# Performance work log

Hardware: AMD Instinct MI355X
Metric: run time of the kernel (lower is better)

Reference implementation:

```python
import jax, jax.numpy as jnp
import numpy as np

B, T, N = 4, 512, 16
D, H = 256, 8
CTS, CN, CE = 6, 4, 3
TSE, AUXE = 192, 64  # TSE + AUXE == D
DK = D // H


def pe_table(L, d):
    # sinusoidal positional encoding (annotated-transformer style)
    pos = jnp.arange(L, dtype=jnp.float32)[:, None]
    div = jnp.exp(jnp.arange(0, d, 2, dtype=jnp.float32) * (-jnp.log(jnp.float32(10000.0)) / d))
    pe = jnp.zeros((L, d), dtype=jnp.float32)
    pe = pe.at[:, 0::2].set(jnp.sin(pos * div)).at[:, 1::2].set(jnp.cos(pos * div))
    return pe


def setup_inputs() -> dict:
    key = jax.random.key(0)
    ks = jax.random.split(key, 32)
    s = 0.02
    inp = {
        'x': jax.random.normal(ks[0], (B, T, D), jnp.float32),
        'masked_data': jax.random.normal(ks[1], (B, N, CTS, T), jnp.float32),
        'node_aux': jax.random.normal(ks[2], (B, N, CN, T), jnp.float32),
        'edge_aux': jax.random.normal(ks[3], (B, N, CE, T), jnp.float32),
        'attention_mask': jax.random.randint(ks[4], (B, T, N * T), 0, 2, jnp.int32),
        # ts branch
        'W_ts1': jax.random.normal(ks[5], (CTS, TSE)) * s, 'b_ts1': jnp.zeros((TSE,)),
        'W_ts2': jax.random.normal(ks[6], (TSE, TSE)) * s, 'b_ts2': jnp.zeros((TSE,)),
        # node aux branch
        'W_a1': jax.random.normal(ks[7], (CN, AUXE)) * s, 'b_a1': jnp.zeros((AUXE,)),
        'W_a2': jax.random.normal(ks[8], (AUXE, AUXE)) * s, 'b_a2': jnp.zeros((AUXE,)),
        # edge branch
        'W_e1': jax.random.normal(ks[9], (CE, D)) * s, 'b_e1': jnp.zeros((D,)),
        'W_e2': jax.random.normal(ks[10], (D, D)) * s, 'b_e2': jnp.zeros((D,)),
        # multi-head cross-attention
        'Wq': jax.random.normal(ks[11], (D, D)) * s, 'bq': jnp.zeros((D,)),
        'Wk': jax.random.normal(ks[12], (D, D)) * s, 'bk': jnp.zeros((D,)),
        'Wv': jax.random.normal(ks[13], (D, D)) * s, 'bv': jnp.zeros((D,)),
        'Wo': jax.random.normal(ks[14], (D, D)) * s, 'bo': jnp.zeros((D,)),
        # sublayer layernorm
        'ln_g': jnp.ones((D,)), 'ln_b': jnp.zeros((D,)),
    }
    return inp


def reference(x, masked_data, node_aux, edge_aux, attention_mask,
              W_ts1, b_ts1, W_ts2, b_ts2, W_a1, b_a1, W_a2, b_a2,
              W_e1, b_e1, W_e2, b_e2, Wq, bq, Wk, bk, Wv, bv, Wo, bo,
              ln_g, ln_b):
    pe = pe_table(T, D)  # [T, D]
    xq = x + pe[None]  # pe applied to query sequence (dropout=identity in eval)

    # per-neighbor ts MLP: transpose [B,N,C,T] -> [B,N,T,C], two Linears with ReLU between
    ts = jax.nn.relu(jnp.einsum('bnct,ce->bnte', masked_data, W_ts1) + b_ts1)
    ts = ts @ W_ts2 + b_ts2  # [B,N,T,TSE]
    aux = jax.nn.relu(jnp.einsum('bnct,ce->bnte', node_aux, W_a1) + b_a1)
    aux = aux @ W_a2 + b_a2  # [B,N,T,AUXE]
    nbr = jnp.concatenate([ts, aux], axis=-1)  # [B,N,T,D]

    edge = jax.nn.relu(jnp.einsum('bnct,cd->bntd', edge_aux, W_e1) + b_e1)
    edge = edge @ W_e2 + b_e2  # [B,N,T,D]

    # PE applied per neighbor (positions restart each neighbor), then concat over kv seq
    keys = (nbr * edge + pe[None, None]).reshape(B, N * T, D)
    vals = (nbr + pe[None, None]).reshape(B, N * T, D)

    # SublayerConnection: xq + attn(LayerNorm(xq), keys, vals, mask)
    mu = xq.mean(-1, keepdims=True)
    var = ((xq - mu) ** 2).mean(-1, keepdims=True)
    xn = (xq - mu) / jnp.sqrt(var + 1e-6) * ln_g + ln_b

    q = (xn @ Wq + bq).reshape(B, T, H, DK).transpose(0, 2, 1, 3)        # [B,H,T,DK]
    k = (keys @ Wk + bk).reshape(B, N * T, H, DK).transpose(0, 2, 1, 3)  # [B,H,NT,DK]
    v = (vals @ Wv + bv).reshape(B, N * T, H, DK).transpose(0, 2, 1, 3)

    scores = jnp.einsum('bhqd,bhkd->bhqk', q, k) / jnp.sqrt(jnp.float32(DK))
    scores = jnp.where(attention_mask[:, None, :, :] == 0, jnp.float32(-1e9), scores)
    attn = jax.nn.softmax(scores, axis=-1)
    ctx = jnp.einsum('bhqk,bhkd->bhqd', attn, v).transpose(0, 2, 1, 3).reshape(B, T, D)
    out = ctx @ Wo + bo
    return xq + out
```

## Files before the change

kernel.cpp:

```cpp
#include <hip/hip_runtime.h>
#include <hip/hip_bf16.h>

#define B_ 4
#define T_ 512
#define N_ 16
#define D_ 256
#define H_ 8
#define DK_ 32
#define NT_ (N_ * T_)
#define CTS_ 6
#define CN_ 4
#define CE_ 3
#define TSE_ 192
#define AUXE_ 64
#define SPLIT_ 8
#define KWORDS_ (NT_ / 64)

#define QSCALE_ 0.1767766952966369f

#define HTS_S 204
#define HAUX_S 76
#define HED_S 268
#define SK_S 268

typedef unsigned long long ull;
typedef unsigned int uint;
typedef __bf16 bf16x8 __attribute__((ext_vector_type(8)));
typedef float f32x4 __attribute__((ext_vector_type(4)));
typedef float f32x16 __attribute__((ext_vector_type(16)));

__global__ __launch_bounds__(256) void pe_kernel(float* pe) {
    int t = blockIdx.x;
    int d = threadIdx.x;
    int j = d >> 1;
    float div = expf((float)(2 * j) * (-9.210340371976184f / 256.0f));
    float a = (float)t * div;
    pe[t * D_ + d] = (d & 1) ? cosf(a) : sinf(a);
}

__global__ __launch_bounds__(256) void maskbits_kernel(const int* __restrict__ mask,
                                                       ull* __restrict__ bitsT) {
    int row = blockIdx.x;
    int b = row >> 9, t = row & (T_ - 1);
    const int* mrow = mask + (size_t)row * NT_;
    int lane = threadIdx.x & 63, wave = threadIdx.x >> 6;
    for (int it = 0; it < NT_ / 256; ++it) {
        int k = it * 256 + wave * 64 + lane;
        ull bal = __ballot(mrow[k] != 0);
        if (lane == 0) bitsT[((size_t)b * KWORDS_ + (k >> 6)) * T_ + t] = bal;
    }
}

__global__ __launch_bounds__(256) void wprep_kernel(
    const float* __restrict__ W_ts1, const float* __restrict__ W_a1,
    const float* __restrict__ W_e1, const float* __restrict__ W_ts2,
    const float* __restrict__ W_a2, const float* __restrict__ W_e2,
    const float* __restrict__ Wk, const float* __restrict__ Wv,
    const float* __restrict__ Wq, const float* __restrict__ Wo,
    __bf16* __restrict__ ts1P, __bf16* __restrict__ a1P, __bf16* __restrict__ e1P,
    __bf16* __restrict__ ts2T, __bf16* __restrict__ a2T, __bf16* __restrict__ e2T,
    __bf16* __restrict__ WkT, __bf16* __restrict__ WvT,
    __bf16* __restrict__ WqT, __bf16* __restrict__ WoT) {
    int i = blockIdx.x * 256 + threadIdx.x;
    if (i < 6144) { int col = i >> 5, k = i & 31;
        ts1P[i] = (__bf16)(k < 6 ? W_ts1[k * TSE_ + col] : 0.f); return; }
    i -= 6144;
    if (i < 2048) { int col = i >> 5, k = i & 31;
        a1P[i] = (__bf16)((k >= 6 && k < 10) ? W_a1[(k - 6) * AUXE_ + col] : 0.f); return; }
    i -= 2048;
    if (i < 8192) { int col = i >> 5, k = i & 31;
        e1P[i] = (__bf16)((k >= 10 && k < 13) ? W_e1[(k - 10) * D_ + col] : 0.f); return; }
    i -= 8192;
    if (i < 36864) {
        int tile = i >> 9, lr = (i >> 5) & 15, kk = i & 31;
        int ct = tile / 6, ks = tile % 6;
        ts2T[i] = (__bf16)W_ts2[(ks * 32 + kk) * TSE_ + ct * 16 + lr]; return; }
    i -= 36864;
    if (i < 4096) {
        int tile = i >> 9, lr = (i >> 5) & 15, kk = i & 31;
        int ct = tile / 2, ks = tile % 2;
        a2T[i] = (__bf16)W_a2[(ks * 32 + kk) * AUXE_ + ct * 16 + lr]; return; }
    i -= 4096;
    if (i < 65536) {
        int tile = i >> 9, lr = (i >> 5) & 15, kk = i & 31;
        int ct = tile >> 3, ks = tile & 7;
        e2T[i] = (__bf16)W_e2[(ks * 32 + kk) * D_ + ct * 16 + lr]; return; }
    i -= 65536;
    if (i < 65536) {
        int tile = i >> 9, lr = (i >> 5) & 15, kk = i & 31;
        int ct = tile >> 3, ks = tile & 7;
        WkT[i] = (__bf16)Wk[(ks * 32 + kk) * D_ + ct * 16 + lr]; return; }
    i -= 65536;
    if (i < 65536) {
        int tile = i >> 9, lr = (i >> 5) & 15, kk = i & 31;
        int ct = tile >> 3, ks = tile & 7;
        WvT[i] = (__bf16)Wv[(ks * 32 + kk) * D_ + ct * 16 + lr]; return; }
    i -= 65536;
    if (i < 65536) {
        int tile = i >> 9, lr = (i >> 5) & 15, kk = i & 31;
        int ct = tile >> 3, ks = tile & 7;
        WqT[i] = (__bf16)(Wq[(ks * 32 + kk) * D_ + ct * 16 + lr] * QSCALE_); return; }
    i -= 65536;
    {
        int tile = i >> 9, lr = (i >> 5) & 15, kk = i & 31;
        int ct = tile >> 3, ks = tile & 7;
        WoT[i] = (__bf16)Wo[(ks * 32 + kk) * D_ + ct * 16 + lr]; }
}

__global__ __launch_bounds__(256, 4) void kv_mfma_kernel(
    const float* __restrict__ md, const float* __restrict__ na, const float* __restrict__ ea,
    const __bf16* __restrict__ ts1P, const __bf16* __restrict__ a1P,
    const __bf16* __restrict__ e1P,
    const float* __restrict__ b_ts1, const float* __restrict__ b_a1,
    const float* __restrict__ b_e1,
    const __bf16* __restrict__ ts2T, const __bf16* __restrict__ a2T,
    const __bf16* __restrict__ e2T,
    const float* __restrict__ b_ts2, const float* __restrict__ b_a2,
    const float* __restrict__ b_e2,
    const __bf16* __restrict__ WkT, const float* __restrict__ bk,
    const __bf16* __restrict__ WvT, const float* __restrict__ bv,
    const float* __restrict__ pe, __bf16* __restrict__ Kb, __bf16* __restrict__ Vf) {
    int blk = blockIdx.x;
    int t0 = (blk & 15) * 32;
    int n = (blk >> 4) & 15;
    int b = blk >> 8;
    int tid = threadIdx.x, lane = tid & 63;
    int wq = tid >> 6;
    int lr = lane & 15, lg = lane >> 4;

    __shared__ __bf16 sA[32 * 40];
    __shared__ __bf16 sU[17536];
    __bf16* hts = sU;
    __bf16* haux = sU + 6528;
    __bf16* hedge = sU + 8960;
    __bf16* skey = sU;
    __bf16* sval = sU + 8576;

    for (int i = tid; i < 32 * 40; i += 256) sA[i] = (__bf16)0.f;
    __syncthreads();
    {
        int t = tid & 31, c0 = tid >> 5;
        size_t bn = (size_t)b * N_ + n;
        for (int c = c0; c < 13; c += 8) {
            float v;
            if (c < 6) v = md[(bn * CTS_ + c) * T_ + t0 + t];
            else if (c < 10) v = na[(bn * CN_ + (c - 6)) * T_ + t0 + t];
            else v = ea[(bn * CE_ + (c - 10)) * T_ + t0 + t];
            sA[t * 40 + c] = (__bf16)v;
        }
    }
    __syncthreads();

    int foff = lr * 32 + lg * 8;
    f32x4 z4 = {0.f, 0.f, 0.f, 0.f};
    bf16x8 a1f0 = *(const bf16x8*)(sA + lr * 40 + lg * 8);
    bf16x8 a1f1 = *(const bf16x8*)(sA + (16 + lr) * 40 + lg * 8);
    int crow0 = lg * 4;

    {
        bool isTs = (wq < 3);
#pragma unroll
        for (int i = 0; i < 4; ++i) {
            int ctn = wq * 4 + i;
            const __bf16* src = isTs ? (ts1P + ctn * 512) : (a1P + (ctn - 12) * 512);
            bf16x8 bf = *(const bf16x8*)(src + foff);
            f32x4 c0 = __builtin_amdgcn_mfma_f32_16x16x32_bf16(a1f0, bf, z4, 0, 0, 0);
            f32x4 c1 = __builtin_amdgcn_mfma_f32_16x16x32_bf16(a1f1, bf, z4, 0, 0, 0);
            if (isTs) {
                int gcol = ctn * 16 + lr;
                float bias = b_ts1[gcol];
#pragma unroll
                for (int r = 0; r < 4; ++r) {
                    hts[(crow0 + r) * HTS_S + gcol] = (__bf16)fmaxf(c0[r] + bias, 0.f);
                    hts[(16 + crow0 + r) * HTS_S + gcol] = (__bf16)fmaxf(c1[r] + bias, 0.f);
                }
            } else {
                int acol = (ctn - 12) * 16 + lr;
                float bias = b_a1[acol];
#pragma unroll
                for (int r = 0; r < 4; ++r) {
                    haux[(crow0 + r) * HAUX_S + acol] = (__bf16)fmaxf(c0[r] + bias, 0.f);
                    haux[(16 + crow0 + r) * HAUX_S + acol] = (__bf16)fmaxf(c1[r] + bias, 0.f);
                }
            }
        }
#pragma unroll
        for (int i = 0; i < 4; ++i) {
            int cte = wq * 4 + i;
            bf16x8 bf = *(const bf16x8*)(e1P + cte * 512 + foff);
            f32x4 c0 = __builtin_amdgcn_mfma_f32_16x16x32_bf16(a1f0, bf, z4, 0, 0, 0);
            f32x4 c1 = __builtin_amdgcn_mfma_f32_16x16x32_bf16(a1f1, bf, z4, 0, 0, 0);
            int gcol = cte * 16 + lr;
            float bias = b_e1[gcol];
#pragma unroll
            for (int r = 0; r < 4; ++r) {
                hedge[(crow0 + r) * HED_S + gcol] = (__bf16)fmaxf(c0[r] + bias, 0.f);
                hedge[(16 + crow0 + r) * HED_S + gcol] = (__bf16)fmaxf(c1[r] + bias, 0.f);
            }
        }
    }
    __syncthreads();

    f32x4 eacc[2][4];
#pragma unroll
    for (int i = 0; i < 4; ++i) { eacc[0][i] = z4; eacc[1][i] = z4; }
    {
        const __bf16* ebase = e2T + (size_t)(wq * 4) * 8 * 512 + foff;
        bf16x8 bcur[4];
#pragma unroll
        for (int i = 0; i < 4; ++i) bcur[i] = *(const bf16x8*)(ebase + i * 4096);
#pragma unroll 1
        for (int ks = 0; ks < 8; ++ks) {
            bf16x8 bnext[4];
            if (ks < 7) {
#pragma unroll
                for (int i = 0; i < 4; ++i)
                    bnext[i] = *(const bf16x8*)(ebase + i * 4096 + (ks + 1) * 512);
            }
            __builtin_amdgcn_sched_barrier(0);
            bf16x8 af0 = *(const bf16x8*)(hedge + lr * HED_S + ks * 32 + lg * 8);
            bf16x8 af1 = *(const bf16x8*)(hedge + (16 + lr) * HED_S + ks * 32 + lg * 8);
#pragma unroll
            for (int i = 0; i < 4; ++i) {
                eacc[0][i] = __builtin_amdgcn_mfma_f32_16x16x32_bf16(af0, bcur[i], eacc[0][i], 0, 0, 0);
                eacc[1][i] = __builtin_amdgcn_mfma_f32_16x16x32_bf16(af1, bcur[i], eacc[1][i], 0, 0, 0);
            }
            if (ks < 7) {
#pragma unroll
                for (int i = 0; i < 4; ++i) bcur[i] = bnext[i];
            }
        }
    }

    f32x4 nacc[2][4];
#pragma unroll
    for (int i = 0; i < 4; ++i) { nacc[0][i] = z4; nacc[1][i] = z4; }
    if (wq < 3) {
        const __bf16* nbase = ts2T + (size_t)(wq * 4) * 6 * 512 + foff;
        bf16x8 bcur[4];
#pragma unroll
        for (int i = 0; i < 4; ++i) bcur[i] = *(const bf16x8*)(nbase + i * 3072);
#pragma unroll 1
        for (int ks = 0; ks < 6; ++ks) {
            bf16x8 bnext[4];
            if (ks < 5) {
#pragma unroll
                for (int i = 0; i < 4; ++i)
                    bnext[i] = *(const bf16x8*)(nbase + i * 3072 + (ks + 1) * 512);
            }
            __builtin_amdgcn_sched_barrier(0);
            bf16x8 af0 = *(const bf16x8*)(hts + lr * HTS_S + ks * 32 + lg * 8);
            bf16x8 af1 = *(const bf16x8*)(hts + (16 + lr) * HTS_S + ks * 32 + lg * 8);
#pragma unroll
            for (int i = 0; i < 4; ++i) {
                nacc[0][i] = __builtin_amdgcn_mfma_f32_16x16x32_bf16(af0, bcur[i], nacc[0][i], 0, 0, 0);
                nacc[1][i] = __builtin_amdgcn_mfma_f32_16x16x32_bf16(af1, bcur[i], nacc[1][i], 0, 0, 0);
            }
            if (ks < 5) {
#pragma unroll
                for (int i = 0; i < 4; ++i) bcur[i] = bnext[i];
            }
        }
    } else {
#pragma unroll
        for (int ks = 0; ks < 2; ++ks) {
            bf16x8 af0 = *(const bf16x8*)(haux + lr * HAUX_S + ks * 32 + lg * 8);
            bf16x8 af1 = *(const bf16x8*)(haux + (16 + lr) * HAUX_S + ks * 32 + lg * 8);
#pragma unroll
            for (int i = 0; i < 4; ++i) {
                bf16x8 bf = *(const bf16x8*)(a2T + (i * 2 + ks) * 512 + foff);
                nacc[0][i] = __builtin_amdgcn_mfma_f32_16x16x32_bf16(af0, bf, nacc[0][i], 0, 0, 0);
                nacc[1][i] = __builtin_amdgcn_mfma_f32_16x16x32_bf16(af1, bf, nacc[1][i], 0, 0, 0);
            }
        }
    }
    __syncthreads();

#pragma unroll
    for (int i = 0; i < 4; ++i) {
        int gcol = wq * 64 + i * 16 + lr;
        float nb_bias = (wq < 3) ? b_ts2[gcol] : b_a2[gcol - 192];
        float ed_bias = b_e2[gcol];
#pragma unroll
        for (int rf = 0; rf < 2; ++rf)
#pragma unroll
            for (int r = 0; r < 4; ++r) {
                int row = rf * 16 + crow0 + r;
                float p = pe[(t0 + row) * D_ + gcol];
                float nb = nacc[rf][i][r] + nb_bias;
                float ed = eacc[rf][i][r] + ed_bias;
                skey[row * SK_S + gcol] = (__bf16)(nb * ed + p);
                sval[row * SK_S + gcol] = (__bf16)(nb + p);
            }
    }
    __syncthreads();

    size_t key0 = (size_t)n * T_ + t0;

    {
        const __bf16* kbse = WkT + (size_t)(wq * 4) * 8 * 512 + foff;
        f32x4 ka[2][4];
#pragma unroll
        for (int i = 0; i < 4; ++i) { ka[0][i] = z4; ka[1][i] = z4; }
        bf16x8 bcur[4];
#pragma unroll
        for (int i = 0; i < 4; ++i) bcur[i] = *(const bf16x8*)(kbse + i * 4096);
#pragma unroll 1
        for (int ks = 0; ks < 8; ++ks) {
            bf16x8 bnext[4];
            if (ks < 7) {
#pragma unroll
                for (int i = 0; i < 4; ++i)
                    bnext[i] = *(const bf16x8*)(kbse + i * 4096 + (ks + 1) * 512);
            }
            __builtin_amdgcn_sched_barrier(0);
            bf16x8 af0 = *(const bf16x8*)(skey + lr * SK_S + ks * 32 + lg * 8);
            bf16x8 af1 = *(const bf16x8*)(skey + (16 + lr) * SK_S + ks * 32 + lg * 8);
#pragma unroll
            for (int i = 0; i < 4; ++i) {
                ka[0][i] = __builtin_amdgcn_mfma_f32_16x16x32_bf16(af0, bcur[i], ka[0][i], 0, 0, 0);
                ka[1][i] = __builtin_amdgcn_mfma_f32_16x16x32_bf16(af1, bcur[i], ka[1][i], 0, 0, 0);
            }
            if (ks < 7) {
#pragma unroll
                for (int i = 0; i < 4; ++i) bcur[i] = bnext[i];
            }
        }
#pragma unroll
        for (int i = 0; i < 4; ++i) {
            int gcol = wq * 64 + i * 16 + lr;
            float kbias = bk[gcol];
            int h = gcol >> 5, dd = gcol & 31;
            size_t bh = (size_t)b * H_ + h;
#pragma unroll
            for (int rf = 0; rf < 2; ++rf) {
                int crow = rf * 16 + crow0;
#pragma unroll
                for (int r = 0; r < 4; ++r)
                    Kb[(bh * NT_ + key0 + crow + r) * DK_ + dd] = (__bf16)(ka[rf][i][r] + kbias);
            }
        }
    }

    {
        const __bf16* vbse = WvT + (size_t)(wq * 4) * 8 * 512 + foff;
        f32x4 va[2][4];
#pragma unroll
        for (int i = 0; i < 4; ++i) { va[0][i] = z4; va[1][i] = z4; }
        bf16x8 bcur[4];
#pragma unroll
        for (int i = 0; i < 4; ++i) bcur[i] = *(const bf16x8*)(vbse + i * 4096);
#pragma unroll 1
        for (int ks = 0; ks < 8; ++ks) {
            bf16x8 bnext[4];
            if (ks < 7) {
#pragma unroll
                for (int i = 0; i < 4; ++i)
                    bnext[i] = *(const bf16x8*)(vbse + i * 4096 + (ks + 1) * 512);
            }
            __builtin_amdgcn_sched_barrier(0);
            bf16x8 af0 = *(const bf16x8*)(sval + lr * SK_S + ks * 32 + lg * 8);
            bf16x8 af1 = *(const bf16x8*)(sval + (16 + lr) * SK_S + ks * 32 + lg * 8);
#pragma unroll
            for (int i = 0; i < 4; ++i) {
                va[0][i] = __builtin_amdgcn_mfma_f32_16x16x32_bf16(af0, bcur[i], va[0][i], 0, 0, 0);
                va[1][i] = __builtin_amdgcn_mfma_f32_16x16x32_bf16(af1, bcur[i], va[1][i], 0, 0, 0);
            }
            if (ks < 7) {
#pragma unroll
                for (int i = 0; i < 4; ++i) bcur[i] = bnext[i];
            }
        }
#pragma unroll
        for (int i = 0; i < 4; ++i) {
            int gcol = wq * 64 + i * 16 + lr;
            float vbias = bv[gcol];
            int h = gcol >> 5, dd = gcol & 31;
            size_t bh = (size_t)b * H_ + h;
#pragma unroll
            for (int rf = 0; rf < 2; ++rf) {
                int crow = rf * 16 + crow0;
                __bf16 tmp[4];
#pragma unroll
                for (int r = 0; r < 4; ++r) tmp[r] = (__bf16)(va[rf][i][r] + vbias);
                size_t kg = key0 + crow;
                int within = (int)(kg & 63);
                int vks = within >> 4, vl5 = (within >> 3) & 1, j0 = within & 7;
                size_t tile = kg >> 6;
                size_t vaddr = ((bh * (NT_ / 64) + tile) * 4 + vks) * 512 +
                               (size_t)(vl5 * 32 + dd) * 8 + j0;
                *(ushort4*)(Vf + vaddr) = *(ushort4*)tmp;
            }
        }
    }
}

__global__ __launch_bounds__(256) void q_mfma_kernel(
    const float* __restrict__ x, const float* __restrict__ pe,
    const __bf16* __restrict__ WqT, const float* __restrict__ bq,
    const float* __restrict__ ln_g, const float* __restrict__ ln_b,
    float* __restrict__ xq, __bf16* __restrict__ Qb) {
    int blk = blockIdx.x;
    int t0 = (blk & 15) * 32;
    int b = blk >> 4;
    int tid = threadIdx.x, lane = tid & 63;
    int wq = tid >> 6, lr = lane & 15, lg = lane >> 4;

    __shared__ __bf16 s_xn[32 * SK_S];

    {
        int row = tid >> 3, sub = tid & 7;
        size_t roff = ((size_t)b * T_ + t0 + row) * D_;
        const float* pr = pe + (t0 + row) * D_;
        f32x4 vv[8];
        float s1 = 0.f, s2 = 0.f;
#pragma unroll
        for (int q4 = 0; q4 < 8; ++q4) {
            int c = q4 * 32 + sub * 4;
            f32x4 xv = *(const f32x4*)(x + roff + c);
            f32x4 pv = *(const f32x4*)(pr + c);
            f32x4 t4;
#pragma unroll
            for (int j = 0; j < 4; ++j) {
                t4[j] = xv[j] + pv[j];
                s1 += t4[j];
                s2 += t4[j] * t4[j];
            }
            *(f32x4*)(xq + roff + c) = t4;
            vv[q4] = t4;
        }
#pragma unroll
        for (int o = 1; o <= 4; o <<= 1) {
            s1 += __shfl_xor(s1, o, 64);
            s2 += __shfl_xor(s2, o, 64);
        }
        float mu = s1 * (1.f / D_);
        float var = s2 * (1.f / D_) - mu * mu;
        float rs = rsqrtf(var + 1e-6f);
#pragma unroll
        for (int q4 = 0; q4 < 8; ++q4) {
            int c = q4 * 32 + sub * 4;
            f32x4 g4 = *(const f32x4*)(ln_g + c);
            f32x4 b4 = *(const f32x4*)(ln_b + c);
#pragma unroll
            for (int j = 0; j < 4; ++j)
                s_xn[row * SK_S + c + j] = (__bf16)((vv[q4][j] - mu) * rs * g4[j] + b4[j]);
        }
    }
    __syncthreads();

    int foff = lr * 32 + lg * 8;
    int crow0 = lg * 4;
    f32x4 z4 = {0.f, 0.f, 0.f, 0.f};
    f32x4 qa[2][4];
#pragma unroll
    for (int i = 0; i < 4; ++i) { qa[0][i] = z4; qa[1][i] = z4; }
    const __bf16* qbse = WqT + (size_t)(wq * 4) * 8 * 512 + foff;
#pragma unroll
    for (int ks = 0; ks < 8; ++ks) {
        bf16x8 af0 = *(const bf16x8*)(s_xn + lr * SK_S + ks * 32 + lg * 8);
        bf16x8 af1 = *(const bf16x8*)(s_xn + (16 + lr) * SK_S + ks * 32 + lg * 8);
#pragma unroll
        for (int i = 0; i < 4; ++i) {
            bf16x8 b8 = *(const bf16x8*)(qbse + i * 4096 + ks * 512);
            qa[0][i] = __builtin_amdgcn_mfma_f32_16x16x32_bf16(af0, b8, qa[0][i], 0, 0, 0);
            qa[1][i] = __builtin_amdgcn_mfma_f32_16x16x32_bf16(af1, b8, qa[1][i], 0, 0, 0);
        }
    }
#pragma unroll
    for (int i = 0; i < 4; ++i) {
        int gcol = wq * 64 + i * 16 + lr;
        float bias = bq[gcol] * QSCALE_;
#pragma unroll
        for (int rf = 0; rf < 2; ++rf)
#pragma unroll
            for (int r = 0; r < 4; ++r)
                Qb[((size_t)b * T_ + t0 + rf * 16 + crow0 + r) * D_ + gcol] =
                    (__bf16)(qa[rf][i][r] + bias);
    }
}

__global__ __launch_bounds__(256, 4) void attn_mfma_kernel(
    const __bf16* __restrict__ Qb, const __bf16* __restrict__ Kb,
    const __bf16* __restrict__ Vf, const ull* __restrict__ bitsT,
    float* __restrict__ Opart, float* __restrict__ Lpart) {
    int blk = blockIdx.x;
    int kh = blk & (SPLIT_ - 1);
    int qt = (blk >> 3) & 3;
    int h = (blk >> 5) & 7;
    int b = blk >> 8;
    int tid = threadIdx.x, lane = tid & 63, w = tid >> 6;
    int lq = lane & 31, l5 = lane >> 5;

    const size_t bh = (size_t)b * H_ + h;
    const int TILES = KWORDS_ / SPLIT_;

    int qglob = qt * 128 + w * 32 + lq;
    const __bf16* qbase = Qb + ((size_t)b * T_ + qglob) * D_ + h * DK_ + l5 * 8;
    bf16x8 qf0 = *(const bf16x8*)(qbase);
    bf16x8 qf1 = *(const bf16x8*)(qbase + 16);

    const __bf16* kp = Kb + bh * NT_ * DK_ + (size_t)(kh * TILES) * 64 * DK_;
    const __bf16* vp = Vf + (bh * (NT_ / 64) + (size_t)(kh * TILES)) * 2048;
    const ull* mp = bitsT + (size_t)b * KWORDS_ * T_ + (size_t)(kh * TILES) * T_ + qglob;

    int k00 = lq * DK_ + l5 * 8;
    int k01 = k00 + 16;
    int k10 = (32 + lq) * DK_ + l5 * 8;
    int k11 = k10 + 16;
    int shamt = 4 * l5;

    f32x16 acc, acc_l, zv;
#pragma unroll
    for (int i = 0; i < 16; ++i) { acc[i] = 0.f; acc_l[i] = 0.f; zv[i] = 0.f; }
    union { uint u[4]; bf16x8 v; } onesf;
    onesf.u[0] = 0x3F803F80u; onesf.u[1] = 0x3F803F80u;
    onesf.u[2] = 0x3F803F80u; onesf.u[3] = 0x3F803F80u;

    bf16x8 kc0 = *(const bf16x8*)(kp + k00);
    bf16x8 kc1 = *(const bf16x8*)(kp + k01);
    bf16x8 kc2 = *(const bf16x8*)(kp + k10);
    bf16x8 kc3 = *(const bf16x8*)(kp + k11);
    ull mw = *mp;

#pragma unroll 1
    for (int kt = 0; kt < TILES; ++kt) {
        bf16x8 vc0 = *(const bf16x8*)(vp + 0 * 512 + lane * 8);
        bf16x8 vc1 = *(const bf16x8*)(vp + 1 * 512 + lane * 8);
        bf16x8 vc2 = *(const bf16x8*)(vp + 2 * 512 + lane * 8);
        bf16x8 vc3 = *(const bf16x8*)(vp + 3 * 512 + lane * 8);
        bf16x8 kn0, kn1, kn2, kn3;
        ull mn = 0;
        if (kt + 1 < TILES) {
            kn0 = *(const bf16x8*)(kp + 2048 + k00);
            kn1 = *(const bf16x8*)(kp + 2048 + k01);
            kn2 = *(const bf16x8*)(kp + 2048 + k10);
            kn3 = *(const bf16x8*)(kp + 2048 + k11);
            mn = mp[T_];
        }
        __builtin_amdgcn_sched_barrier(0);

        ull sh = mw >> shamt;

#pragma unroll
        for (int s = 0; s < 2; ++s) {
            f32x16 sc = __builtin_amdgcn_mfma_f32_32x32x16_bf16(
                s ? kc2 : kc0, qf0, zv, 0, 0, 0);
            sc = __builtin_amdgcn_mfma_f32_32x32x16_bf16(
                s ? kc3 : kc1, qf1, sc, 0, 0, 0);

            uint ms = (uint)(sh >> (32 * s));
            float p[16];
#pragma unroll
            for (int r = 0; r < 16; ++r) {
                int pos = (r & 3) + 8 * (r >> 2);
                float e = __expf(sc[r]);
                int mb = __builtin_amdgcn_sbfe((int)ms, (uint)pos, 1u);
                p[r] = __uint_as_float(__float_as_uint(e) & (uint)mb);
            }

#pragma unroll
            for (int h2 = 0; h2 < 2; ++h2) {
                uint w0, w1, w2, w3;
                asm("v_cvt_pk_bf16_f32 %0, %1, %2" : "=v"(w0) : "v"(p[8 * h2 + 0]), "v"(p[8 * h2 + 1]));
                asm("v_cvt_pk_bf16_f32 %0, %1, %2" : "=v"(w1) : "v"(p[8 * h2 + 2]), "v"(p[8 * h2 + 3]));
                asm("v_cvt_pk_bf16_f32 %0, %1, %2" : "=v"(w2) : "v"(p[8 * h2 + 4]), "v"(p[8 * h2 + 5]));
                asm("v_cvt_pk_bf16_f32 %0, %1, %2" : "=v"(w3) : "v"(p[8 * h2 + 6]), "v"(p[8 * h2 + 7]));
                asm volatile("v_permlane32_swap_b32 %0, %1" : "+v"(w0), "+v"(w2));
                asm volatile("v_permlane32_swap_b32 %0, %1" : "+v"(w1), "+v"(w3));
                union { uint u[4]; bf16x8 v; } pa;
                pa.u[0] = w0; pa.u[1] = w1; pa.u[2] = w2; pa.u[3] = w3;
                bf16x8 vfr = (s == 0) ? (h2 == 0 ? vc0 : vc1) : (h2 == 0 ? vc2 : vc3);
                acc = __builtin_amdgcn_mfma_f32_32x32x16_bf16(pa.v, vfr, acc, 0, 0, 0);
                acc_l = __builtin_amdgcn_mfma_f32_32x32x16_bf16(pa.v, onesf.v, acc_l, 0, 0, 0);
            }
        }

        kp += 2048;
        vp += 2048;
        mp += T_;
        if (kt + 1 < TILES) {
            kc0 = kn0; kc1 = kn1; kc2 = kn2; kc3 = kn3;
            mw = mn;
        }
    }

    size_t obase = (((size_t)kh * B_ + b) * H_ + h) * T_ + qt * 128 + w * 32;
#pragma unroll
    for (int r = 0; r < 16; ++r) {
        int q = (r & 3) + 8 * (r >> 2) + 4 * l5;
        Opart[(obase + q) * DK_ + lq] = acc[r];
    }
    if (lq == 0) {
#pragma unroll
        for (int r = 0; r < 16; ++r) {
            int q = (r & 3) + 8 * (r >> 2) + 4 * l5;
            Lpart[obase + q] = acc_l[r];
        }
    }
}

__global__ __launch_bounds__(256) void merge_kernel(
    const float* __restrict__ Opart, const float* __restrict__ Lpart,
    __bf16* __restrict__ ctxb) {
    int idx = blockIdx.x * 256 + threadIdx.x;
    int d = idx & 31;
    int t = (idx >> 5) & (T_ - 1);
    int bh = idx >> 14;
    int h = bh & 7, b = bh >> 3;
    size_t ps = (size_t)B_ * H_ * T_;
    size_t base = (size_t)bh * T_ + t;
    float L = 0.f, o = 0.f;
#pragma unroll
    for (int s = 0; s < SPLIT_; ++s) {
        L += Lpart[s * ps + base];
        o += Opart[(s * ps + base) * DK_ + d];
    }
    ctxb[((size_t)b * T_ + t) * D_ + h * DK_ + d] = (__bf16)(o / L);
}

__global__ __launch_bounds__(256) void out_mfma_kernel(
    const __bf16* __restrict__ ctxb, const float* __restrict__ xq,
    const __bf16* __restrict__ WoT, const float* __restrict__ bo,
    float* __restrict__ out) {
    int blk = blockIdx.x;
    int t0 = (blk & 15) * 32;
    int b = blk >> 4;
    int tid = threadIdx.x, lane = tid & 63;
    int wq = tid >> 6, lr = lane & 15, lg = lane >> 4;

    __shared__ __bf16 sc_[32 * SK_S];
    for (int idx = tid; idx < 32 * 64; idx += 256) {
        int r = idx >> 6, c4 = (idx & 63) * 4;
        *(ushort4*)(sc_ + r * SK_S + c4) =
            *(const ushort4*)(ctxb + ((size_t)b * T_ + t0 + r) * D_ + c4);
    }
    __syncthreads();

    int foff = lr * 32 + lg * 8;
    int crow0 = lg * 4;
    f32x4 z4 = {0.f, 0.f, 0.f, 0.f};
    f32x4 oa[2][4];
#pragma unroll
    for (int i = 0; i < 4; ++i) { oa[0][i] = z4; oa[1][i] = z4; }
    const __bf16* obse = WoT + (size_t)(wq * 4) * 8 * 512 + foff;
#pragma unroll
    for (int ks = 0; ks < 8; ++ks) {
        bf16x8 af0 = *(const bf16x8*)(sc_ + lr * SK_S + ks * 32 + lg * 8);
        bf16x8 af1 = *(const bf16x8*)(sc_ + (16 + lr) * SK_S + ks * 32 + lg * 8);
#pragma unroll
        for (int i = 0; i < 4; ++i) {
            bf16x8 b8 = *(const bf16x8*)(obse + i * 4096 + ks * 512);
            oa[0][i] = __builtin_amdgcn_mfma_f32_16x16x32_bf16(af0, b8, oa[0][i], 0, 0, 0);
            oa[1][i] = __builtin_amdgcn_mfma_f32_16x16x32_bf16(af1, b8, oa[1][i], 0, 0, 0);
        }
    }
#pragma unroll
    for (int i = 0; i < 4; ++i) {
        int gcol = wq * 64 + i * 16 + lr;
        float bias = bo[gcol];
#pragma unroll
        for (int rf = 0; rf < 2; ++rf)
#pragma unroll
            for (int r = 0; r < 4; ++r) {
                size_t off = ((size_t)b * T_ + t0 + rf * 16 + crow0 + r) * D_ + gcol;
                out[off] = xq[off] + oa[rf][i][r] + bias;
            }
    }
}

extern "C" void kernel_launch(void* const* d_in, const int* in_sizes, int n_in,
                              void* d_out, int out_size, void* d_ws, size_t ws_size,
                              hipStream_t stream) {
    const float* x = (const float*)d_in[0];
    const float* md = (const float*)d_in[1];
    const float* na = (const float*)d_in[2];
    const float* ea = (const float*)d_in[3];
    const int* mask = (const int*)d_in[4];
    const float* W_ts1 = (const float*)d_in[5];
    const float* b_ts1 = (const float*)d_in[6];
    const float* W_ts2 = (const float*)d_in[7];
    const float* b_ts2 = (const float*)d_in[8];
    const float* W_a1 = (const float*)d_in[9];
    const float* b_a1 = (const float*)d_in[10];
    const float* W_a2 = (const float*)d_in[11];
    const float* b_a2 = (const float*)d_in[12];
    const float* W_e1 = (const float*)d_in[13];
    const float* b_e1 = (const float*)d_in[14];
    const float* W_e2 = (const float*)d_in[15];
    const float* b_e2 = (const float*)d_in[16];
    const float* Wq = (const float*)d_in[17];
    const float* bq = (const float*)d_in[18];
    const float* Wk = (const float*)d_in[19];
    const float* bk = (const float*)d_in[20];
    const float* Wv = (const float*)d_in[21];
    const float* bv = (const float*)d_in[22];
    const float* Wo = (const float*)d_in[23];
    const float* bo = (const float*)d_in[24];
    const float* ln_g = (const float*)d_in[25];
    const float* ln_b = (const float*)d_in[26];
    float* out = (float*)d_out;

    char* ws = (char*)d_ws;
    float* pe = (float*)ws;     ws += (size_t)T_ * D_ * 4;
    ull* bitsT = (ull*)ws;      ws += (size_t)B_ * KWORDS_ * T_ * 8;
    __bf16* Kb = (__bf16*)ws;   ws += (size_t)B_ * H_ * NT_ * DK_ * 2;
    __bf16* Vf = (__bf16*)ws;   ws += (size_t)B_ * H_ * NT_ * DK_ * 2;
    float* xq = (float*)ws;     ws += (size_t)B_ * T_ * D_ * 4;
    __bf16* Qb = (__bf16*)ws;   ws += (size_t)B_ * T_ * D_ * 2;
    __bf16* ctxb = (__bf16*)ws; ws += (size_t)B_ * T_ * D_ * 2;
    float* Opart = (float*)ws;  ws += (size_t)SPLIT_ * B_ * H_ * T_ * DK_ * 4;
    float* Lpart = (float*)ws;  ws += (size_t)SPLIT_ * B_ * H_ * T_ * 4;
    __bf16* ts1P = (__bf16*)ws; ws += 6144 * 2;
    __bf16* a1P = (__bf16*)ws;  ws += 2048 * 2;
    __bf16* e1P = (__bf16*)ws;  ws += 8192 * 2;
    __bf16* ts2T = (__bf16*)ws; ws += 36864 * 2;
    __bf16* a2T = (__bf16*)ws;  ws += 4096 * 2;
    __bf16* e2T = (__bf16*)ws;  ws += 65536 * 2;
    __bf16* WkT = (__bf16*)ws;  ws += 65536 * 2;
    __bf16* WvT = (__bf16*)ws;  ws += 65536 * 2;
    __bf16* WqT = (__bf16*)ws;  ws += 65536 * 2;
    __bf16* WoT = (__bf16*)ws;  ws += 65536 * 2;

    pe_kernel<<<T_, 256, 0, stream>>>(pe);
    maskbits_kernel<<<B_ * T_, 256, 0, stream>>>(mask, bitsT);
    wprep_kernel<<<1504, 256, 0, stream>>>(W_ts1, W_a1, W_e1, W_ts2, W_a2, W_e2,
                                           Wk, Wv, Wq, Wo,
                                           ts1P, a1P, e1P, ts2T, a2T, e2T,
                                           WkT, WvT, WqT, WoT);
    kv_mfma_kernel<<<B_ * N_ * (T_ / 32), 256, 0, stream>>>(
        md, na, ea, ts1P, a1P, e1P, b_ts1, b_a1, b_e1,
        ts2T, a2T, e2T, b_ts2, b_a2, b_e2, WkT, bk, WvT, bv, pe, Kb, Vf);
    q_mfma_kernel<<<B_ * (T_ / 32), 256, 0, stream>>>(x, pe, WqT, bq, ln_g, ln_b, xq, Qb);
    attn_mfma_kernel<<<B_ * H_ * (T_ / 128) * SPLIT_, 256, 0, stream>>>(
        Qb, Kb, Vf, bitsT, Opart, Lpart);
    merge_kernel<<<(B_ * H_ * T_ * DK_) / 256, 256, 0, stream>>>(Opart, Lpart, ctxb);
    out_mfma_kernel<<<B_ * (T_ / 32), 256, 0, stream>>>(ctxb, xq, WoT, bo, out);
}
```

Before: 125.3 us.

## Precompute mask as fragment-ordered bf16 halfword masks and recompute xq in epilogue

Replaces the packed 1-bit-per-key mask with a 32-bit-per-key-pair mask laid out in the attention MFMA fragment order. The inner loop can then mask the packed bf16 probabilities with a plain AND instead of per-element bit extraction on the fp32 values. The mask buffer grows about sixteenfold and is re-read by every head, which adds a lot of memory and cache traffic. Separately, the xq buffer is dropped and the output epilogue recomputes x + pe directly.

```diff
diff --git a/kernel.cpp b/kernel.cpp
--- a/kernel.cpp
+++ b/kernel.cpp
@@ -14,7 +14,6 @@
 #define TSE_ 192
 #define AUXE_ 64
 #define SPLIT_ 8
-#define KWORDS_ (NT_ / 64)
 
 #define QSCALE_ 0.1767766952966369f
 
@@ -28,6 +27,7 @@
 typedef __bf16 bf16x8 __attribute__((ext_vector_type(8)));
 typedef float f32x4 __attribute__((ext_vector_type(4)));
 typedef float f32x16 __attribute__((ext_vector_type(16)));
+typedef uint uint4v __attribute__((ext_vector_type(4)));
 
 __global__ __launch_bounds__(256) void pe_kernel(float* pe) {
     int t = blockIdx.x;
@@ -38,17 +38,23 @@
     pe[t * D_ + d] = (d & 1) ? cosf(a) : sinf(a);
 }
 
-__global__ __launch_bounds__(256) void maskbits_kernel(const int* __restrict__ mask,
-                                                       ull* __restrict__ bitsT) {
-    int row = blockIdx.x;
-    int b = row >> 9, t = row & (T_ - 1);
-    const int* mrow = mask + (size_t)row * NT_;
-    int lane = threadIdx.x & 63, wave = threadIdx.x >> 6;
-    for (int it = 0; it < NT_ / 256; ++it) {
-        int k = it * 256 + wave * 64 + lane;
-        ull bal = __ballot(mrow[k] != 0);
-        if (lane == 0) bitsT[((size_t)b * KWORDS_ + (k >> 6)) * T_ + t] = bal;
-    }
+__global__ __launch_bounds__(256) void maskwords_kernel(const int* __restrict__ mask,
+                                                        uint* __restrict__ Mf) {
+    int i = blockIdx.x * 256 + threadIdx.x;
+    int j = i & 3;
+    int l5 = (i >> 2) & 1;
+    int lq = (i >> 3) & 31;
+    int h2 = (i >> 8) & 1;
+    int s = (i >> 9) & 1;
+    int tile = (i >> 10) & 127;
+    int w = (i >> 17) & 3;
+    int qt = (i >> 19) & 3;
+    int b = i >> 21;
+    int q = qt * 128 + w * 32 + lq;
+    int k0 = tile * 64 + s * 32 + h2 * 16 + l5 * 8 + 2 * j;
+    const int* mrow = mask + ((size_t)b * T_ + q) * NT_ + k0;
+    uint wd = (mrow[0] ? 0x0000FFFFu : 0u) | (mrow[1] ? 0xFFFF0000u : 0u);
+    Mf[i] = wd;
 }
 
 __global__ __launch_bounds__(256) void wprep_kernel(
@@ -399,7 +405,7 @@
     const float* __restrict__ x, const float* __restrict__ pe,
     const __bf16* __restrict__ WqT, const float* __restrict__ bq,
     const float* __restrict__ ln_g, const float* __restrict__ ln_b,
-    float* __restrict__ xq, __bf16* __restrict__ Qb) {
+    __bf16* __restrict__ Qb) {
     int blk = blockIdx.x;
     int t0 = (blk & 15) * 32;
     int b = blk >> 4;
@@ -426,7 +432,6 @@
                 s1 += t4[j];
                 s2 += t4[j] * t4[j];
             }
-            *(f32x4*)(xq + roff + c) = t4;
             vv[q4] = t4;
         }
 #pragma unroll
@@ -482,7 +487,7 @@
 
 __global__ __launch_bounds__(256, 4) void attn_mfma_kernel(
     const __bf16* __restrict__ Qb, const __bf16* __restrict__ Kb,
-    const __bf16* __restrict__ Vf, const ull* __restrict__ bitsT,
+    const __bf16* __restrict__ Vf, const uint* __restrict__ Mf,
     float* __restrict__ Opart, float* __restrict__ Lpart) {
     int blk = blockIdx.x;
     int kh = blk & (SPLIT_ - 1);
@@ -493,7 +498,7 @@
     int lq = lane & 31, l5 = lane >> 5;
 
     const size_t bh = (size_t)b * H_ + h;
-    const int TILES = KWORDS_ / SPLIT_;
+    const int TILES = (NT_ / 64) / SPLIT_;
 
     int qglob = qt * 128 + w * 32 + lq;
     const __bf16* qbase = Qb + ((size_t)b * T_ + qglob) * D_ + h * DK_ + l5 * 8;
@@ -502,13 +507,13 @@
 
     const __bf16* kp = Kb + bh * NT_ * DK_ + (size_t)(kh * TILES) * 64 * DK_;
     const __bf16* vp = Vf + (bh * (NT_ / 64) + (size_t)(kh * TILES)) * 2048;
-    const ull* mp = bitsT + (size_t)b * KWORDS_ * T_ + (size_t)(kh * TILES) * T_ + qglob;
+    const uint* mp = Mf + ((((size_t)b * 4 + qt) * 4 + w) * 128 + kh * TILES) * 1024
+                        + lq * 8 + l5 * 4;
 
     int k00 = lq * DK_ + l5 * 8;
     int k01 = k00 + 16;
     int k10 = (32 + lq) * DK_ + l5 * 8;
     int k11 = k10 + 16;
-    int shamt = 4 * l5;
 
     f32x16 acc, acc_l, zv;
 #pragma unroll
@@ -521,7 +526,6 @@
     bf16x8 kc1 = *(const bf16x8*)(kp + k01);
     bf16x8 kc2 = *(const bf16x8*)(kp + k10);
     bf16x8 kc3 = *(const bf16x8*)(kp + k11);
-    ull mw = *mp;
 
 #pragma unroll 1
     for (int kt = 0; kt < TILES; ++kt) {
@@ -529,18 +533,18 @@
         bf16x8 vc1 = *(const bf16x8*)(vp + 1 * 512 + lane * 8);
         bf16x8 vc2 = *(const bf16x8*)(vp + 2 * 512 + lane * 8);
         bf16x8 vc3 = *(const bf16x8*)(vp + 3 * 512 + lane * 8);
+        uint4v mf00 = *(const uint4v*)(mp + 0 * 256);
+        uint4v mf01 = *(const uint4v*)(mp + 1 * 256);
+        uint4v mf10 = *(const uint4v*)(mp + 2 * 256);
+        uint4v mf11 = *(const uint4v*)(mp + 3 * 256);
         bf16x8 kn0, kn1, kn2, kn3;
-        ull mn = 0;
         if (kt + 1 < TILES) {
             kn0 = *(const bf16x8*)(kp + 2048 + k00);
             kn1 = *(const bf16x8*)(kp + 2048 + k01);
             kn2 = *(const bf16x8*)(kp + 2048 + k10);
             kn3 = *(const bf16x8*)(kp + 2048 + k11);
-            mn = mp[T_];
         }
         __builtin_amdgcn_sched_barrier(0);
-
-        ull sh = mw >> shamt;
 
 #pragma unroll
         for (int s = 0; s < 2; ++s) {
@@ -549,18 +553,13 @@
             sc = __builtin_amdgcn_mfma_f32_32x32x16_bf16(
                 s ? kc3 : kc1, qf1, sc, 0, 0, 0);
 
-            uint ms = (uint)(sh >> (32 * s));
             float p[16];
 #pragma unroll
-            for (int r = 0; r < 16; ++r) {
-                int pos = (r & 3) + 8 * (r >> 2);
-                float e = __expf(sc[r]);
-                int mb = __builtin_amdgcn_sbfe((int)ms, (uint)pos, 1u);
-                p[r] = __uint_as_float(__float_as_uint(e) & (uint)mb);
-            }
+            for (int r = 0; r < 16; ++r) p[r] = __expf(sc[r]);
 
 #pragma unroll
             for (int h2 = 0; h2 < 2; ++h2) {
+                uint4v mfr = (s == 0) ? (h2 == 0 ? mf00 : mf01) : (h2 == 0 ? mf10 : mf11);
                 uint w0, w1, w2, w3;
                 asm("v_cvt_pk_bf16_f32 %0, %1, %2" : "=v"(w0) : "v"(p[8 * h2 + 0]), "v"(p[8 * h2 + 1]));
                 asm("v_cvt_pk_bf16_f32 %0, %1, %2" : "=v"(w1) : "v"(p[8 * h2 + 2]), "v"(p[8 * h2 + 3]));
@@ -569,7 +568,10 @@
                 asm volatile("v_permlane32_swap_b32 %0, %1" : "+v"(w0), "+v"(w2));
                 asm volatile("v_permlane32_swap_b32 %0, %1" : "+v"(w1), "+v"(w3));
                 union { uint u[4]; bf16x8 v; } pa;
-                pa.u[0] = w0; pa.u[1] = w1; pa.u[2] = w2; pa.u[3] = w3;
+                pa.u[0] = w0 & mfr[0];
+                pa.u[1] = w1 & mfr[1];
+                pa.u[2] = w2 & mfr[2];
+                pa.u[3] = w3 & mfr[3];
                 bf16x8 vfr = (s == 0) ? (h2 == 0 ? vc0 : vc1) : (h2 == 0 ? vc2 : vc3);
                 acc = __builtin_amdgcn_mfma_f32_32x32x16_bf16(pa.v, vfr, acc, 0, 0, 0);
                 acc_l = __builtin_amdgcn_mfma_f32_32x32x16_bf16(pa.v, onesf.v, acc_l, 0, 0, 0);
@@ -578,10 +580,9 @@
 
         kp += 2048;
         vp += 2048;
-        mp += T_;
+        mp += 1024;
         if (kt + 1 < TILES) {
             kc0 = kn0; kc1 = kn1; kc2 = kn2; kc3 = kn3;
-            mw = mn;
         }
     }
 
@@ -620,9 +621,9 @@
 }
 
 __global__ __launch_bounds__(256) void out_mfma_kernel(
-    const __bf16* __restrict__ ctxb, const float* __restrict__ xq,
-    const __bf16* __restrict__ WoT, const float* __restrict__ bo,
-    float* __restrict__ out) {
+    const __bf16* __restrict__ ctxb, const float* __restrict__ x,
+    const float* __restrict__ pe, const __bf16* __restrict__ WoT,
+    const float* __restrict__ bo, float* __restrict__ out) {
     int blk = blockIdx.x;
     int t0 = (blk & 15) * 32;
     int b = blk >> 4;
@@ -663,8 +664,9 @@
         for (int rf = 0; rf < 2; ++rf)
 #pragma unroll
             for (int r = 0; r < 4; ++r) {
-                size_t off = ((size_t)b * T_ + t0 + rf * 16 + crow0 + r) * D_ + gcol;
-                out[off] = xq[off] + oa[rf][i][r] + bias;
+                int t = t0 + rf * 16 + crow0 + r;
+                size_t off = ((size_t)b * T_ + t) * D_ + gcol;
+                out[off] = x[off] + pe[t * D_ + gcol] + oa[rf][i][r] + bias;
             }
     }
 }
@@ -703,10 +705,9 @@
 
     char* ws = (char*)d_ws;
     float* pe = (float*)ws;     ws += (size_t)T_ * D_ * 4;
-    ull* bitsT = (ull*)ws;      ws += (size_t)B_ * KWORDS_ * T_ * 8;
+    uint* Mf = (uint*)ws;       ws += (size_t)B_ * T_ * (NT_ / 2) * 4;
     __bf16* Kb = (__bf16*)ws;   ws += (size_t)B_ * H_ * NT_ * DK_ * 2;
     __bf16* Vf = (__bf16*)ws;   ws += (size_t)B_ * H_ * NT_ * DK_ * 2;
-    float* xq = (float*)ws;     ws += (size_t)B_ * T_ * D_ * 4;
     __bf16* Qb = (__bf16*)ws;   ws += (size_t)B_ * T_ * D_ * 2;
     __bf16* ctxb = (__bf16*)ws; ws += (size_t)B_ * T_ * D_ * 2;
     float* Opart = (float*)ws;  ws += (size_t)SPLIT_ * B_ * H_ * T_ * DK_ * 4;
@@ -723,7 +724,7 @@
     __bf16* WoT = (__bf16*)ws;  ws += 65536 * 2;
 
     pe_kernel<<<T_, 256, 0, stream>>>(pe);
-    maskbits_kernel<<<B_ * T_, 256, 0, stream>>>(mask, bitsT);
+    maskwords_kernel<<<(B_ * T_ * (NT_ / 2)) / 256, 256, 0, stream>>>(mask, Mf);
     wprep_kernel<<<1504, 256, 0, stream>>>(W_ts1, W_a1, W_e1, W_ts2, W_a2, W_e2,
                                            Wk, Wv, Wq, Wo,
                                            ts1P, a1P, e1P, ts2T, a2T, e2T,
@@ -731,9 +732,9 @@
     kv_mfma_kernel<<<B_ * N_ * (T_ / 32), 256, 0, stream>>>(
         md, na, ea, ts1P, a1P, e1P, b_ts1, b_a1, b_e1,
         ts2T, a2T, e2T, b_ts2, b_a2, b_e2, WkT, bk, WvT, bv, pe, Kb, Vf);
-    q_mfma_kernel<<<B_ * (T_ / 32), 256, 0, stream>>>(x, pe, WqT, bq, ln_g, ln_b, xq, Qb);
+    q_mfma_kernel<<<B_ * (T_ / 32), 256, 0, stream>>>(x, pe, WqT, bq, ln_g, ln_b, Qb);
     attn_mfma_kernel<<<B_ * H_ * (T_ / 128) * SPLIT_, 256, 0, stream>>>(
-        Qb, Kb, Vf, bitsT, Opart, Lpart);
+        Qb, Kb, Vf, Mf, Opart, Lpart);
     merge_kernel<<<(B_ * H_ * T_ * DK_) / 256, 256, 0, stream>>>(Opart, Lpart, ctxb);
-    out_mfma_kernel<<<B_ * (T_ / 32), 256, 0, stream>>>(ctxb, xq, WoT, bo, out);
-}
+    out_mfma_kernel<<<B_ * (T_ / 32), 256, 0, stream>>>(ctxb, x, pe, WoT, bo, out);
+}
```

Measured after the change: 143.0 us. 14.1% more time.
